# Performance work log

Hardware: AMD Instinct MI355X
Metric: run time of the kernel (lower is better)

The kernel has to match this reference:

```python
import jax, jax.numpy as jnp
import numpy as np

SIGMA_HS = jnp.array([5.0, 10.0, 20.0, 40.0], dtype=jnp.float32)  # one sigma per head


def gaussian_prior(n_heads, len_q, len_k):
    # Lower-triangular Gaussian positional bias: exp(-(j-i)^2 / (2*sigma_h^2)) for i>=j, else 0
    i = jnp.arange(len_q)[:, None]
    j = jnp.arange(len_k)[None, :]
    diff2 = (j - i).astype(jnp.float32) ** 2                      # [Lq, Lk]
    sig2 = 2.0 * SIGMA_HS[:n_heads, None, None] ** 2              # [H, 1, 1]
    gm = jnp.exp(-diff2[None, :, :] / sig2)                       # [H, Lq, Lk]
    return jnp.where((i >= j)[None, :, :], gm, 0.0)


def setup_inputs() -> dict:
    key = jax.random.key(0)
    kq, kk, kv = jax.random.split(key, 3)
    B, H, S, D = 4, 4, 2048, 128
    Q = jax.random.normal(kq, (B, H, S, D), dtype=jnp.float32)
    K = jax.random.normal(kk, (B, H, S, D), dtype=jnp.float32)
    V = jax.random.normal(kv, (B, H, S, D), dtype=jnp.float32)
    # causal mask: True = masked out (matches masked_fill_ semantics)
    causal = ~jnp.tril(jnp.ones((S, S), dtype=bool))
    attn_mask = jnp.broadcast_to(causal[None, None, :, :], (B, H, S, S))
    return {"Q": Q, "K": K, "V": V, "attn_mask": attn_mask}


def reference(Q, K, V, attn_mask):
    B, H, Lq, Dk = Q.shape
    Lk = K.shape[2]
    scores = jnp.einsum("bhqd,bhkd->bhqk", Q, K) / jnp.sqrt(jnp.float32(Dk))
    scores = scores + gaussian_prior(H, Lq, Lk)[None]             # broadcast over batch
    scores = jnp.where(attn_mask, -1e9, scores)
    attn = jax.nn.softmax(scores, axis=-1)
    context = jnp.einsum("bhqk,bhkd->bhqd", attn, V)
    return context
```

## Files before the change

kernel.cpp:

```cpp
#include <hip/hip_runtime.h>
#include <hip/hip_bf16.h>

typedef __bf16 bf16;
typedef __bf16 bf16x2 __attribute__((ext_vector_type(2)));
typedef __bf16 bf16x4 __attribute__((ext_vector_type(4)));
typedef __bf16 bf16x8 __attribute__((ext_vector_type(8)));
typedef float f32x16 __attribute__((ext_vector_type(16)));
typedef unsigned uint2v __attribute__((ext_vector_type(2)));

#define S_LEN 2048
#define DHEAD 128
#define QBLK 32
#define KVBLK 64
#define TILE_E 8192

#define LOG2E 1.4426950408889634f
#define SCALE2 (0.08838834764831845f * 1.4426950408889634f)
#define CLOG 0.52876637f
#define MFIX 16.0f

#define EXP2F(x) __builtin_amdgcn_exp2f(x)

__global__ void prep(const float* __restrict__ K, const float* __restrict__ V,
                     bf16* __restrict__ Kf, bf16* __restrict__ Vf) {
  __shared__ bf16 Vl[64][136];
  const int tid = threadIdx.x;
  const int bh = blockIdx.x;
  const int t  = blockIdx.y;
  const float* Kp = K + ((size_t)bh * S_LEN + t * 64) * DHEAD;
  const float* Vp = V + ((size_t)bh * S_LEN + t * 64) * DHEAD;
  bf16* Kout = Kf + ((size_t)bh * 32 + t) * TILE_E;
  bf16* Vout = Vf + ((size_t)bh * 32 + t) * TILE_E;

#pragma unroll
  for (int it = 0; it < 4; ++it) {
    int idx = it * 256 + tid;
    int row = idx >> 4, ch = idx & 15;
    float4 a = *(const float4*)(Vp + row * DHEAD + ch * 8);
    float4 b = *(const float4*)(Vp + row * DHEAD + ch * 8 + 4);
    bf16x8 f;
    f[0] = (bf16)a.x; f[1] = (bf16)a.y; f[2] = (bf16)a.z; f[3] = (bf16)a.w;
    f[4] = (bf16)b.x; f[5] = (bf16)b.y; f[6] = (bf16)b.z; f[7] = (bf16)b.w;
    *(bf16x8*)&Vl[row][ch * 8] = f;
  }

#pragma unroll
  for (int it = 0; it < 4; ++it) {
    int c = it * 256 + tid;
    int grp = c >> 9, dc = (c >> 6) & 7, l = (c >> 1) & 31, hi = c & 1;
    const float* src = Kp + (grp * 32 + l) * DHEAD + dc * 16 + hi * 8;
    float4 a = *(const float4*)src;
    float4 b = *(const float4*)(src + 4);
    bf16x8 f;
    f[0] = (bf16)a.x; f[1] = (bf16)a.y; f[2] = (bf16)a.z; f[3] = (bf16)a.w;
    f[4] = (bf16)b.x; f[5] = (bf16)b.y; f[6] = (bf16)b.z; f[7] = (bf16)b.w;
    *(bf16x8*)(Kout + (size_t)c * 8) = f;
  }
  __syncthreads();

#pragma unroll
  for (int it = 0; it < 4; ++it) {
    int c = it * 256 + tid;
    int db = c >> 8, ks = (c >> 6) & 3, l = (c >> 1) & 31, hi = c & 1;
    int s0 = ks * 16 + hi * 8, d = db * 32 + l;
    bf16x8 f;
#pragma unroll
    for (int e = 0; e < 8; ++e) f[e] = Vl[s0 + e][d];
    *(bf16x8*)(Vout + (size_t)c * 8) = f;
  }
}

__device__ inline unsigned pack2(float a, float b) {
  union { bf16x2 h; unsigned u; } cv;
  cv.h[0] = (bf16)a; cv.h[1] = (bf16)b;
  return cv.u;
}

__launch_bounds__(256, 2)
__global__ void gpsdp_attn(const float* __restrict__ Q,
                           const bf16* __restrict__ Kb,
                           const bf16* __restrict__ Vb,
                           float* __restrict__ Out) {
  __shared__ float obuf[2][64][68];
  __shared__ float lbuf[2][64];

  const int tid  = threadIdx.x;
  const int par  = tid >> 6;
  const int lane = tid & 63;
  const int ql   = lane & 31;
  const int hi   = lane >> 5;

  const int bh = blockIdx.x;
  const int h  = bh & 3;
  const int qt = 63 - blockIdx.y;
  const int q0 = qt * QBLK;
  const int q  = q0 + ql;

  const float inv2sig2_tab[4] = {0.02f, 0.005f, 0.00125f, 0.0003125f};
  const float biasc2 = inv2sig2_tab[h] * LOG2E;

  const float* Qp = Q + (size_t)bh * S_LEN * DHEAD;
  float*       Op = Out + (size_t)bh * S_LEN * DHEAD;
  const bf16* Kt0 = Kb + (size_t)bh * 32 * TILE_E + (ql * 2 + hi) * 8;
  const bf16* Vt0 = Vb + (size_t)bh * 32 * TILE_E + (ql * 2 + hi) * 8;

  int   crow_i[16];
  float crow_f[16];
#pragma unroll
  for (int r = 0; r < 16; ++r) {
    crow_i[r] = (r & 3) + 8 * (r >> 2) + 4 * hi;
    crow_f[r] = (float)crow_i[r];
  }

  bf16x8 qB[8];
  {
    const float* qrow = Qp + (size_t)q * DHEAD;
#pragma unroll
    for (int dc = 0; dc < 8; ++dc) {
      const float* p = qrow + dc * 16 + hi * 8;
      float4 a = *(const float4*)p;
      float4 b = *(const float4*)(p + 4);
      bf16x8 f;
      f[0] = (bf16)a.x; f[1] = (bf16)a.y; f[2] = (bf16)a.z; f[3] = (bf16)a.w;
      f[4] = (bf16)b.x; f[5] = (bf16)b.y; f[6] = (bf16)b.z; f[7] = (bf16)b.w;
      qB[dc] = f;
    }
  }

  float l_run = 0.f;
  f32x16 accO[4];
#pragma unroll
  for (int db = 0; db < 4; ++db)
#pragma unroll
    for (int r = 0; r < 16; ++r) accO[db][r] = 0.f;

  const int ntiles = qt / 2 + 1;
  for (int t = par; t < ntiles; t += 4) {
    const int kb = t * KVBLK;
    const bf16* Kt = Kt0 + (size_t)t * TILE_E;
    const bf16* Vt = Vt0 + (size_t)t * TILE_E;

    f32x16 sS[2];
    __builtin_amdgcn_s_setprio(1);
#pragma unroll
    for (int grp = 0; grp < 2; ++grp) {
      f32x16 acc;
#pragma unroll
      for (int r = 0; r < 16; ++r) acc[r] = 0.f;
#pragma unroll
      for (int dc = 0; dc < 8; ++dc) {
        bf16x8 af = *(const bf16x8*)(Kt + grp * 4096 + dc * 512);
        acc = __builtin_amdgcn_mfma_f32_32x32x16_bf16(af, qB[dc], acc, 0, 0, 0);
      }
      sS[grp] = acc;
    }
    __builtin_amdgcn_s_setprio(0);

    bf16x8 vfr[16];
#pragma unroll
    for (int db = 0; db < 4; ++db)
#pragma unroll
      for (int ks = 0; ks < 4; ++ks)
        vfr[db * 4 + ks] = *(const bf16x8*)(Vt + db * 2048 + ks * 512);

    float ps[4] = {0.f, 0.f, 0.f, 0.f};
    unsigned pw[2][8];
    const bool far = (kb + 383 < q0);
    if (far) {
#pragma unroll
      for (int grp = 0; grp < 2; ++grp) {
#pragma unroll
        for (int r = 0; r < 16; ++r) {
          float p = EXP2F(fmaf(sS[grp][r], SCALE2, -MFIX));
          ps[r & 3] += p;
          sS[grp][r] = p;
        }
#pragma unroll
        for (int jj = 0; jj < 4; ++jj) {
          pw[grp][2 * jj]     = pack2(sS[grp][4 * jj],     sS[grp][4 * jj + 1]);
          pw[grp][2 * jj + 1] = pack2(sS[grp][4 * jj + 2], sS[grp][4 * jj + 3]);
        }
      }
    } else {
      const float fq = (float)(q - kb);
#pragma unroll
      for (int grp = 0; grp < 2; ++grp) {
#pragma unroll
        for (int r = 0; r < 16; ++r) {
          float d = fq - (float)(grp * 32) - crow_f[r];
          float bias2 = EXP2F(fmaf(d * d, -biasc2, CLOG));
          float s2 = fmaf(sS[grp][r], SCALE2, bias2 - MFIX);
          float p = (d >= 0.f) ? EXP2F(s2) : 0.0f;
          ps[r & 3] += p;
          sS[grp][r] = p;
        }
#pragma unroll
        for (int jj = 0; jj < 4; ++jj) {
          pw[grp][2 * jj]     = pack2(sS[grp][4 * jj],     sS[grp][4 * jj + 1]);
          pw[grp][2 * jj + 1] = pack2(sS[grp][4 * jj + 2], sS[grp][4 * jj + 3]);
        }
      }
    }
    l_run += (ps[0] + ps[1]) + (ps[2] + ps[3]);

    bf16x8 pf[4];
#pragma unroll
    for (int grp = 0; grp < 2; ++grp) {
#pragma unroll
      for (int s = 0; s < 2; ++s) {
        uint2v r0 = __builtin_amdgcn_permlane32_swap(pw[grp][4 * s + 0], pw[grp][4 * s + 2], false, false);
        uint2v r1 = __builtin_amdgcn_permlane32_swap(pw[grp][4 * s + 1], pw[grp][4 * s + 3], false, false);
        union { uint4 wd; bf16x8 v; } u;
        u.wd.x = r0[0]; u.wd.y = r1[0]; u.wd.z = r0[1]; u.wd.w = r1[1];
        pf[grp * 2 + s] = u.v;
      }
    }

    __builtin_amdgcn_s_setprio(1);
#pragma unroll
    for (int db = 0; db < 4; ++db) {
#pragma unroll
      for (int ks = 0; ks < 4; ++ks) {
        accO[db] = __builtin_amdgcn_mfma_f32_32x32x16_bf16(pf[ks], vfr[db * 4 + ks], accO[db], 0, 0, 0);
      }
    }
    __builtin_amdgcn_s_setprio(0);
  }

  auto publish = [&](int slot) {
    lbuf[slot][lane] = l_run;
#pragma unroll
    for (int db = 0; db < 4; ++db)
#pragma unroll
      for (int r4 = 0; r4 < 4; ++r4) {
        float4 v = make_float4(accO[db][r4 * 4], accO[db][r4 * 4 + 1],
                               accO[db][r4 * 4 + 2], accO[db][r4 * 4 + 3]);
        *(float4*)&obuf[slot][lane][db * 16 + r4 * 4] = v;
      }
  };
  auto merge_from = [&](int slot) {
    l_run += lbuf[slot][lane];
#pragma unroll
    for (int db = 0; db < 4; ++db) {
#pragma unroll
      for (int r4 = 0; r4 < 4; ++r4) {
        float4 o1 = *(const float4*)&obuf[slot][lane][db * 16 + r4 * 4];
        accO[db][r4 * 4 + 0] += o1.x;
        accO[db][r4 * 4 + 1] += o1.y;
        accO[db][r4 * 4 + 2] += o1.z;
        accO[db][r4 * 4 + 3] += o1.w;
      }
    }
  };

  if (par == 1) publish(0);
  if (par == 3) publish(1);
  __syncthreads();
  if (par == 0) merge_from(0);
  if (par == 2) { merge_from(1); publish(1); }
  __syncthreads();
  if (par == 0) {
    merge_from(1);

    float l_tot = l_run + __shfl_xor(l_run, 32);
    float invl = 1.0f / l_tot;
    float iv[16];
#pragma unroll
    for (int r = 0; r < 16; ++r) iv[r] = __shfl(invl, crow_i[r]);
#pragma unroll
    for (int db = 0; db < 4; ++db) {
#pragma unroll
      for (int r = 0; r < 16; ++r) {
        Op[(size_t)(q0 + crow_i[r]) * DHEAD + db * 32 + ql] = accO[db][r] * iv[r];
      }
    }
  }
}

extern "C" void kernel_launch(void* const* d_in, const int* in_sizes, int n_in,
                              void* d_out, int out_size, void* d_ws, size_t ws_size,
                              hipStream_t stream) {
  const float* Q = (const float*)d_in[0];
  const float* K = (const float*)d_in[1];
  const float* V = (const float*)d_in[2];
  float* Out = (float*)d_out;

  bf16* Kf = (bf16*)d_ws;
  bf16* Vf = (bf16*)d_ws + (size_t)16 * S_LEN * DHEAD;

  prep<<<dim3(16, 32), 256, 0, stream>>>(K, V, Kf, Vf);

  dim3 grid(16, 64);
  gpsdp_attn<<<grid, 256, 0, stream>>>(Q, Kf, Vf, Out);
}
```

Before: 53.03 us.

## Prefetch next K tile into LDS via async global_load_lds per wave

```diff
diff --git a/kernel.cpp b/kernel.cpp
--- a/kernel.cpp
+++ b/kernel.cpp
@@ -76,12 +76,18 @@
   return cv.u;
 }
 
+__device__ inline void gload_lds16(const bf16* gsrc, char* ldst) {
+  __builtin_amdgcn_global_load_lds(
+      (const __attribute__((address_space(1))) void*)gsrc,
+      (__attribute__((address_space(3))) void*)ldst, 16, 0, 0);
+}
+
 __launch_bounds__(256, 2)
 __global__ void gpsdp_attn(const float* __restrict__ Q,
                            const bf16* __restrict__ Kb,
                            const bf16* __restrict__ Vb,
                            float* __restrict__ Out) {
-  __shared__ float obuf[2][64][68];
+  __shared__ __align__(16) char smem_raw[65536];
   __shared__ float lbuf[2][64];
 
   const int tid  = threadIdx.x;
@@ -103,6 +109,9 @@
   float*       Op = Out + (size_t)bh * S_LEN * DHEAD;
   const bf16* Kt0 = Kb + (size_t)bh * 32 * TILE_E + (ql * 2 + hi) * 8;
   const bf16* Vt0 = Vb + (size_t)bh * 32 * TILE_E + (ql * 2 + hi) * 8;
+
+  char* kst_raw = smem_raw + par * 16384;
+  const bf16* kst = (const bf16*)kst_raw;
 
   int   crow_i[16];
   float crow_f[16];
@@ -135,10 +144,27 @@
     for (int r = 0; r < 16; ++r) accO[db][r] = 0.f;
 
   const int ntiles = qt / 2 + 1;
+
+  if (par < ntiles) {
+    const bf16* Ksrc = Kt0 + (size_t)par * TILE_E;
+#pragma unroll
+    for (int c = 0; c < 16; ++c)
+      gload_lds16(Ksrc + c * 512, kst_raw + c * 1024);
+  }
+
   for (int t = par; t < ntiles; t += 4) {
     const int kb = t * KVBLK;
-    const bf16* Kt = Kt0 + (size_t)t * TILE_E;
     const bf16* Vt = Vt0 + (size_t)t * TILE_E;
+
+    asm volatile("s_waitcnt vmcnt(0)" ::: "memory");
+    __builtin_amdgcn_sched_barrier(0);
+
+    bf16x8 vfr[16];
+#pragma unroll
+    for (int db = 0; db < 4; ++db)
+#pragma unroll
+      for (int ks = 0; ks < 4; ++ks)
+        vfr[db * 4 + ks] = *(const bf16x8*)(Vt + db * 2048 + ks * 512);
 
     f32x16 sS[2];
     __builtin_amdgcn_s_setprio(1);
@@ -149,19 +175,24 @@
       for (int r = 0; r < 16; ++r) acc[r] = 0.f;
 #pragma unroll
       for (int dc = 0; dc < 8; ++dc) {
-        bf16x8 af = *(const bf16x8*)(Kt + grp * 4096 + dc * 512);
+        bf16x8 af = *(const bf16x8*)&kst[(grp * 8 + dc) * 512 + lane * 8];
         acc = __builtin_amdgcn_mfma_f32_32x32x16_bf16(af, qB[dc], acc, 0, 0, 0);
       }
       sS[grp] = acc;
     }
     __builtin_amdgcn_s_setprio(0);
 
-    bf16x8 vfr[16];
-#pragma unroll
-    for (int db = 0; db < 4; ++db)
-#pragma unroll
-      for (int ks = 0; ks < 4; ++ks)
-        vfr[db * 4 + ks] = *(const bf16x8*)(Vt + db * 2048 + ks * 512);
+    asm volatile("s_waitcnt lgkmcnt(0)" ::: "memory");
+    __builtin_amdgcn_sched_barrier(0);
+    {
+      const int tn = t + 4;
+      if (tn < ntiles) {
+        const bf16* Ksrc = Kt0 + (size_t)tn * TILE_E;
+#pragma unroll
+        for (int c = 0; c < 16; ++c)
+          gload_lds16(Ksrc + c * 512, kst_raw + c * 1024);
+      }
+    }
 
     float ps[4] = {0.f, 0.f, 0.f, 0.f};
     unsigned pw[2][8];
@@ -227,6 +258,10 @@
     __builtin_amdgcn_s_setprio(0);
   }
 
+  asm volatile("s_waitcnt vmcnt(0)" ::: "memory");
+  __syncthreads();
+  float* obuf = (float*)smem_raw;
+
   auto publish = [&](int slot) {
     lbuf[slot][lane] = l_run;
 #pragma unroll
@@ -235,7 +270,7 @@
       for (int r4 = 0; r4 < 4; ++r4) {
         float4 v = make_float4(accO[db][r4 * 4], accO[db][r4 * 4 + 1],
                                accO[db][r4 * 4 + 2], accO[db][r4 * 4 + 3]);
-        *(float4*)&obuf[slot][lane][db * 16 + r4 * 4] = v;
+        *(float4*)&obuf[(slot * 64 + lane) * 68 + db * 16 + r4 * 4] = v;
       }
   };
   auto merge_from = [&](int slot) {
@@ -244,7 +279,7 @@
     for (int db = 0; db < 4; ++db) {
 #pragma unroll
       for (int r4 = 0; r4 < 4; ++r4) {
-        float4 o1 = *(const float4*)&obuf[slot][lane][db * 16 + r4 * 4];
+        float4 o1 = *(const float4*)&obuf[(slot * 64 + lane) * 68 + db * 16 + r4 * 4];
         accO[db][r4 * 4 + 0] += o1.x;
         accO[db][r4 * 4 + 1] += o1.y;
         accO[db][r4 * 4 + 2] += o1.z;
```

Measured after the change: 54.83 us. +3.4%, slower.
